# Performance work log

Hardware: AMD Instinct MI355X
Metric: run time of the kernel (lower is better)

Reference implementation:

```python
import jax, jax.numpy as jnp
import numpy as np

OUT_FEAT = 32  # output_feature; projected dim = OUT_FEAT**2 = 1024
D_K = OUT_FEAT ** 0.5  # NOTE: source divides by sqrt(output_feature), not sqrt(output_feature^2)


def setup_inputs() -> dict:
    key = jax.random.key(0)
    ks = jax.random.split(key, 7)
    N, D_in, D_proj = 4096, 1024, OUT_FEAT * OUT_FEAT
    s = 1.0 / np.sqrt(D_in)
    return {
        "x": jax.random.normal(ks[0], (N, D_in), jnp.float32),
        "Wq": jax.random.normal(ks[1], (D_in, D_proj), jnp.float32) * s,
        "bq": jax.random.normal(ks[2], (D_proj,), jnp.float32) * s,
        "Wk": jax.random.normal(ks[3], (D_in, D_proj), jnp.float32) * s,
        "bk": jax.random.normal(ks[4], (D_proj,), jnp.float32) * s,
        "Wv": jax.random.normal(ks[5], (D_in, D_proj), jnp.float32) * s,
        "bv": jax.random.normal(ks[6], (D_proj,), jnp.float32) * s,
    }


def reference(x, Wq, bq, Wk, bk, Wv, bv):
    # QKV projections: [N, D_proj]
    Q = x @ Wq + bq
    K = x @ Wk + bk
    V = x @ Wv + bv
    # scores: [N, N], scaled by sqrt(output_feature) per the source
    scores = (Q @ K.T) / D_K
    attn_weights = jax.nn.softmax(scores, axis=-1)
    attn_output = attn_weights @ V  # [N, D_proj]
    attn_output = attn_output.reshape(-1, OUT_FEAT, OUT_FEAT)  # mode='cov' reshape
    return attn_output, attn_weights
```

## Files before the change

### kernel.cpp

```cpp
#include <hip/hip_runtime.h>

typedef short short8 __attribute__((ext_vector_type(8)));
typedef float f32x4 __attribute__((ext_vector_type(4)));

constexpr int NROW  = 4096;
constexpr int DIN   = 1024;
constexpr int DPROJ = 1024;
constexpr float INV_DK = 0.17677669529663687f;

__device__ __forceinline__ unsigned short f2bf(float f) {
  union { float f; unsigned int u; } v; v.f = f;
  unsigned int r = v.u + 0x7FFFu + ((v.u >> 16) & 1u);
  return (unsigned short)(r >> 16);
}
__device__ __forceinline__ float bf2f(unsigned short h) {
  union { unsigned int u; float f; } v; v.u = ((unsigned int)h) << 16; return v.f;
}

template<int KB>
__device__ __forceinline__ void stage_tile(const unsigned short* __restrict__ g,
                                           long row0, long ldK, long k0,
                                           unsigned short* lds_tile, int w, int lane) {
  if constexpr (KB == 64) {
    const int rsub = lane >> 3;
    const int csw  = ((lane & 7) ^ (rsub & 7)) * 8;
#pragma unroll
    for (int it = 0; it < 4; ++it) {
      const int rowblk = w * 32 + it * 8;
      const unsigned short* src = g + (row0 + rowblk + rsub) * ldK + k0 + csw;
      unsigned short* dst = lds_tile + rowblk * 64;
      __builtin_amdgcn_global_load_lds(
          (const __attribute__((address_space(1))) unsigned int*)(const void*)src,
          (__attribute__((address_space(3))) unsigned int*)(void*)dst, 16, 0, 0);
    }
  } else {
    const int rsub = lane >> 2;
    const int csw  = ((lane & 3) ^ ((rsub >> 1) & 3)) * 8;
#pragma unroll
    for (int it = 0; it < 2; ++it) {
      const int rowblk = w * 32 + it * 16;
      const unsigned short* src = g + (row0 + rowblk + rsub) * ldK + k0 + csw;
      unsigned short* dst = lds_tile + rowblk * 32;
      __builtin_amdgcn_global_load_lds(
          (const __attribute__((address_space(1))) unsigned int*)(const void*)src,
          (__attribute__((address_space(3))) unsigned int*)(void*)dst, 16, 0, 0);
    }
  }
}

__device__ __forceinline__ void stage_tile64r(const unsigned short* __restrict__ g,
                                              long row0, long ldK, long k0,
                                              unsigned short* lds_tile, int w, int lane) {
  const int rsub = lane >> 3;
  const int csw  = ((lane & 7) ^ (rsub & 7)) * 8;
#pragma unroll
  for (int it = 0; it < 2; ++it) {
    const int rowblk = w * 16 + it * 8;
    const unsigned short* src = g + (row0 + rowblk + rsub) * ldK + k0 + csw;
    unsigned short* dst = lds_tile + rowblk * 64;
    __builtin_amdgcn_global_load_lds(
        (const __attribute__((address_space(1))) unsigned int*)(const void*)src,
        (__attribute__((address_space(3))) unsigned int*)(void*)dst, 16, 0, 0);
  }
}

__global__ __launch_bounds__(256, 2) void qk_proj(
    const unsigned short* __restrict__ xh, const unsigned short* __restrict__ xl,
    const unsigned short* __restrict__ WqTh, const unsigned short* __restrict__ WqTl,
    const unsigned short* __restrict__ WkTh, const unsigned short* __restrict__ WkTl,
    const float* __restrict__ bq, const float* __restrict__ bk,
    unsigned short* __restrict__ Qh, unsigned short* __restrict__ Ql,
    unsigned short* __restrict__ Kh, unsigned short* __restrict__ Kl)
{
  constexpr int K = 1024, N = 1024, TS = 128 * 32;
  __shared__ __align__(16) unsigned short lds[2][4 * TS];
  const int tid = threadIdx.x, w = tid >> 6, lane = tid & 63;
  const int wr = w >> 1, wc = w & 1, lrow = lane & 15, lgrp = lane >> 4;
  const int which = blockIdx.x >> 8;
  const int b = blockIdx.x & 255;
  const long bm = (long)(b >> 3) * 128;
  const long bn = (long)(b & 7) * 128;
  const unsigned short* Bh = which ? WkTh : WqTh;
  const unsigned short* Bl = which ? WkTl : WqTl;
  const float* bias = which ? bk : bq;
  unsigned short* Oh = which ? Kh : Qh;
  unsigned short* Ol = which ? Kl : Ql;

  f32x4 acc[4][4] = {};
  const int nsteps = K >> 5;

  stage_tile<32>(xh, bm, K, 0, &lds[0][0 * TS], w, lane);
  stage_tile<32>(Bh, bn, K, 0, &lds[0][1 * TS], w, lane);
  stage_tile<32>(xl, bm, K, 0, &lds[0][2 * TS], w, lane);
  stage_tile<32>(Bl, bn, K, 0, &lds[0][3 * TS], w, lane);

  int cur = 0;
  for (int t = 0; t < nsteps; ++t) {
    __syncthreads();
    if (t + 1 < nsteps) {
      const long k0 = (long)(t + 1) << 5;
      const int nb = cur ^ 1;
      stage_tile<32>(xh, bm, K, k0, &lds[nb][0 * TS], w, lane);
      stage_tile<32>(Bh, bn, K, k0, &lds[nb][1 * TS], w, lane);
      stage_tile<32>(xl, bm, K, k0, &lds[nb][2 * TS], w, lane);
      stage_tile<32>(Bl, bn, K, k0, &lds[nb][3 * TS], w, lane);
    }
    const unsigned short* L = lds[cur];
    short8 ah[4], bh[4], al[4], bl[4];
#pragma unroll
    for (int i = 0; i < 4; ++i) {
      const int ra = wr * 64 + i * 16 + lrow;
      const int offa = ra * 32 + ((lgrp ^ ((ra >> 1) & 3)) * 8);
      ah[i] = *(const short8*)&L[0 * TS + offa];
      al[i] = *(const short8*)&L[2 * TS + offa];
      const int rb = wc * 64 + i * 16 + lrow;
      const int offb = rb * 32 + ((lgrp ^ ((rb >> 1) & 3)) * 8);
      bh[i] = *(const short8*)&L[1 * TS + offb];
      bl[i] = *(const short8*)&L[3 * TS + offb];
    }
#pragma unroll
    for (int i = 0; i < 4; ++i)
#pragma unroll
      for (int j = 0; j < 4; ++j) {
        acc[i][j] = __builtin_amdgcn_mfma_f32_16x16x32_bf16(ah[i], bh[j], acc[i][j], 0, 0, 0);
        acc[i][j] = __builtin_amdgcn_mfma_f32_16x16x32_bf16(ah[i], bl[j], acc[i][j], 0, 0, 0);
        acc[i][j] = __builtin_amdgcn_mfma_f32_16x16x32_bf16(al[i], bh[j], acc[i][j], 0, 0, 0);
      }
    cur ^= 1;
  }

#pragma unroll
  for (int i = 0; i < 4; ++i) {
    const long rbase = bm + wr * 64 + i * 16 + lgrp * 4;
#pragma unroll
    for (int j = 0; j < 4; ++j) {
      const long cg = bn + wc * 64 + j * 16 + lrow;
#pragma unroll
      for (int r = 0; r < 4; ++r) {
        const long rg = rbase + r;
        float v = acc[i][j][r] + bias[cg];
        unsigned short h = f2bf(v);
        Oh[rg * N + cg] = h;
        Ol[rg * N + cg] = f2bf(v - bf2f(h));
      }
    }
  }
}

template<int EPI>
__global__ __launch_bounds__(256, 2) void gemm_n64(
    const unsigned short* __restrict__ A, const unsigned short* __restrict__ B,
    const float* __restrict__ bias, float* __restrict__ Cf,
    unsigned short* __restrict__ Co, int M, int N, int K)
{
  constexpr int TSA = 128 * 64;
  constexpr int TSB = 64 * 64;
  __shared__ __align__(16) unsigned short lds[2][TSA + TSB];
  const int tid = threadIdx.x, w = tid >> 6, lane = tid & 63;
  const int wr = w >> 1, wc = w & 1, lrow = lane & 15, lgrp = lane >> 4;
  const long bm = (long)blockIdx.y * 128, bn = (long)blockIdx.x * 64;

  f32x4 acc[4][2] = {};
  const int nsteps = K >> 6;

  stage_tile<64>(A, bm, K, 0, &lds[0][0], w, lane);
  stage_tile64r(B, bn, K, 0, &lds[0][TSA], w, lane);

  int cur = 0;
  for (int t = 0; t < nsteps; ++t) {
    __syncthreads();
    if (t + 1 < nsteps) {
      const long k0 = (long)(t + 1) << 6;
      const int nb = cur ^ 1;
      stage_tile<64>(A, bm, K, k0, &lds[nb][0], w, lane);
      stage_tile64r(B, bn, K, k0, &lds[nb][TSA], w, lane);
    }
    const unsigned short* L = lds[cur];
#pragma unroll
    for (int s = 0; s < 2; ++s) {
      short8 a[4], bb[2];
#pragma unroll
      for (int i = 0; i < 4; ++i) {
        const int ra = wr * 64 + i * 16 + lrow;
        const int offa = ra * 64 + (((s * 4 + lgrp) ^ (ra & 7)) * 8);
        a[i] = *(const short8*)&L[offa];
      }
#pragma unroll
      for (int j = 0; j < 2; ++j) {
        const int rb = wc * 32 + j * 16 + lrow;
        const int offb = rb * 64 + (((s * 4 + lgrp) ^ (rb & 7)) * 8);
        bb[j] = *(const short8*)&L[TSA + offb];
      }
#pragma unroll
      for (int i = 0; i < 4; ++i)
#pragma unroll
        for (int j = 0; j < 2; ++j)
          acc[i][j] = __builtin_amdgcn_mfma_f32_16x16x32_bf16(a[i], bb[j], acc[i][j], 0, 0, 0);
    }
    cur ^= 1;
  }

#pragma unroll
  for (int i = 0; i < 4; ++i) {
    const long rbase = bm + wr * 64 + i * 16 + lgrp * 4;
#pragma unroll
    for (int j = 0; j < 2; ++j) {
      const long cg = bn + wc * 32 + j * 16 + lrow;
#pragma unroll
      for (int r = 0; r < 4; ++r) {
        const long rg = rbase + r;
        if constexpr (EPI == 0) {
          Cf[rg * (long)N + cg] = acc[i][j][r];
        } else {
          Co[rg * (long)N + cg] = f2bf(acc[i][j][r] + bias[rg]);
        }
      }
    }
  }
}

__device__ __forceinline__ void stage256(const unsigned short* __restrict__ g,
    long row0, long ldK, long k0, unsigned short* tile, int w, int lane, int rnd)
{
  const int row_in = rnd * 128 + w * 16 + (lane >> 2);
  const int csw = ((lane & 3) ^ ((row_in >> 1) & 3)) * 8;
  const unsigned short* src = g + (row0 + row_in) * ldK + k0 + csw;
  unsigned short* dst = tile + (rnd * 128 + w * 16) * 32;
  __builtin_amdgcn_global_load_lds(
      (const __attribute__((address_space(1))) unsigned int*)(const void*)src,
      (__attribute__((address_space(3))) unsigned int*)(void*)dst, 16, 0, 0);
}

__global__ __launch_bounds__(512, 2) void score_gemm256(
    const unsigned short* __restrict__ Ah, const unsigned short* __restrict__ Al,
    const unsigned short* __restrict__ Bh, const unsigned short* __restrict__ Bl,
    float* __restrict__ Cf, int M, int N, int K, float alpha)
{
  __shared__ __align__(16) unsigned short lds[2][4 * 8192];
  const int tid  = threadIdx.x;
  const int w    = tid >> 6, lane = tid & 63;
  const int wr   = w >> 2,   wc   = w & 3;
  const int lrow = lane & 15, lgrp = lane >> 4;
  const long bm = (long)blockIdx.y * 256, bn = (long)blockIdx.x * 256;

  f32x4 acc[8][4] = {};
  const int nsteps = K >> 5;

  {
    unsigned short* B0 = &lds[0][0];
#pragma unroll
    for (int r = 0; r < 2; ++r) {
      stage256(Ah, bm, K, 0, B0 + 0 * 8192, w, lane, r);
      stage256(Al, bm, K, 0, B0 + 1 * 8192, w, lane, r);
      stage256(Bh, bn, K, 0, B0 + 2 * 8192, w, lane, r);
      stage256(Bl, bn, K, 0, B0 + 3 * 8192, w, lane, r);
    }
  }
  asm volatile("s_waitcnt vmcnt(0)" ::: "memory");

  int cur = 0;
  for (int t = 0; t < nsteps; ++t) {
    const unsigned short* L = &lds[cur][0];
    unsigned short* Ln = &lds[cur ^ 1][0];
    const long kn = (long)(t + 1) << 5;
    const bool pf = (t + 1 < nsteps);
#pragma unroll
    for (int q = 0; q < 4; ++q) {
      __builtin_amdgcn_s_barrier();
      __builtin_amdgcn_sched_barrier(0);
      const int mh = q >> 1, nh = q & 1;
      short8 a_h[4], a_l[4], b_h[2], b_l[2];
#pragma unroll
      for (int i = 0; i < 4; ++i) {
        const int ra = wr * 128 + mh * 64 + i * 16 + lrow;
        const int offa = ra * 32 + ((lgrp ^ ((ra >> 1) & 3)) * 8);
        a_h[i] = *(const short8*)&L[0 * 8192 + offa];
        a_l[i] = *(const short8*)&L[1 * 8192 + offa];
      }
#pragma unroll
      for (int j = 0; j < 2; ++j) {
        const int rb = wc * 64 + nh * 32 + j * 16 + lrow;
        const int offb = rb * 32 + ((lgrp ^ ((rb >> 1) & 3)) * 8);
        b_h[j] = *(const short8*)&L[2 * 8192 + offb];
        b_l[j] = *(const short8*)&L[3 * 8192 + offb];
      }
      if (pf && q == 0) {
#pragma unroll
        for (int r = 0; r < 2; ++r) {
          stage256(Ah, bm, K, kn, Ln + 0 * 8192, w, lane, r);
          stage256(Bh, bn, K, kn, Ln + 2 * 8192, w, lane, r);
        }
      }
      if (pf && q == 1) {
#pragma unroll
        for (int r = 0; r < 2; ++r) {
          stage256(Al, bm, K, kn, Ln + 1 * 8192, w, lane, r);
          stage256(Bl, bn, K, kn, Ln + 3 * 8192, w, lane, r);
        }
      }
      __builtin_amdgcn_sched_barrier(0);
      __builtin_amdgcn_s_setprio(1);
#pragma unroll
      for (int i = 0; i < 4; ++i)
#pragma unroll
        for (int j = 0; j < 2; ++j) {
          const int ai = mh * 4 + i, aj = nh * 2 + j;
          acc[ai][aj] = __builtin_amdgcn_mfma_f32_16x16x32_bf16(a_h[i], b_h[j], acc[ai][aj], 0, 0, 0);
          acc[ai][aj] = __builtin_amdgcn_mfma_f32_16x16x32_bf16(a_h[i], b_l[j], acc[ai][aj], 0, 0, 0);
          acc[ai][aj] = __builtin_amdgcn_mfma_f32_16x16x32_bf16(a_l[i], b_h[j], acc[ai][aj], 0, 0, 0);
        }
      __builtin_amdgcn_s_setprio(0);
      if (q == 3) {
        asm volatile("s_waitcnt vmcnt(0)" ::: "memory");
        __builtin_amdgcn_sched_barrier(0);
      }
    }
    cur ^= 1;
  }

#pragma unroll
  for (int i = 0; i < 8; ++i) {
    const long rbase = bm + wr * 128 + i * 16 + lgrp * 4;
#pragma unroll
    for (int j = 0; j < 4; ++j) {
      const long cg = bn + wc * 64 + j * 16 + lrow;
#pragma unroll
      for (int r = 0; r < 4; ++r)
        Cf[(rbase + r) * (long)N + cg] = alpha * acc[i][j][r];
    }
  }
}

__global__ __launch_bounds__(256) void split_rows(const float* __restrict__ in,
    unsigned short* __restrict__ oh, unsigned short* __restrict__ ol, int n4)
{
  int idx = blockIdx.x * 256 + threadIdx.x;
  const int stride = gridDim.x * 256;
  for (; idx < n4; idx += stride) {
    float4 v = ((const float4*)in)[idx];
    ushort4 h, l;
    h.x = f2bf(v.x); l.x = f2bf(v.x - bf2f(h.x));
    h.y = f2bf(v.y); l.y = f2bf(v.y - bf2f(h.y));
    h.z = f2bf(v.z); l.z = f2bf(v.z - bf2f(h.z));
    h.w = f2bf(v.w); l.w = f2bf(v.w - bf2f(h.w));
    ((ushort4*)oh)[idx] = h;
    ((ushort4*)ol)[idx] = l;
  }
}

__global__ __launch_bounds__(256) void split_transpose(const float* __restrict__ W,
    unsigned short* __restrict__ oTh, unsigned short* __restrict__ oTl, int R, int C)
{
  __shared__ float t[64][65];
  const int rt = blockIdx.y * 64, ct = blockIdx.x * 64;
  const int r0 = threadIdx.x >> 4, c4 = (threadIdx.x & 15) * 4;
#pragma unroll
  for (int rr = 0; rr < 4; ++rr) {
    const int row = r0 + rr * 16;
    float4 v = *(const float4*)(W + (long)(rt + row) * C + ct + c4);
    t[row][c4 + 0] = v.x; t[row][c4 + 1] = v.y;
    t[row][c4 + 2] = v.z; t[row][c4 + 3] = v.w;
  }
  __syncthreads();
#pragma unroll
  for (int rr = 0; rr < 4; ++rr) {
    const int orow = r0 + rr * 16;
    float x0 = t[c4 + 0][orow], x1 = t[c4 + 1][orow];
    float x2 = t[c4 + 2][orow], x3 = t[c4 + 3][orow];
    ushort4 h, l;
    h.x = f2bf(x0); l.x = f2bf(x0 - bf2f(h.x));
    h.y = f2bf(x1); l.y = f2bf(x1 - bf2f(h.y));
    h.z = f2bf(x2); l.z = f2bf(x2 - bf2f(h.z));
    h.w = f2bf(x3); l.w = f2bf(x3 - bf2f(h.w));
    *(ushort4*)(oTh + (long)(ct + orow) * R + rt + c4) = h;
    *(ushort4*)(oTl + (long)(ct + orow) * R + rt + c4) = l;
  }
}

__global__ __launch_bounds__(256) void softmax_p(float* __restrict__ S,
                                                 unsigned short* __restrict__ P)
{
  const int tid = threadIdx.x;
  float* p = S + (size_t)blockIdx.x * 4096;
  unsigned short* pb = P + (size_t)blockIdx.x * 4096;
  float4 v[4];
  float mx = -3.402823466e38f;
#pragma unroll
  for (int i = 0; i < 4; ++i) {
    v[i] = *(const float4*)(p + 4 * (tid + i * 256));
    mx = fmaxf(mx, fmaxf(fmaxf(v[i].x, v[i].y), fmaxf(v[i].z, v[i].w)));
  }
#pragma unroll
  for (int off = 32; off >= 1; off >>= 1) mx = fmaxf(mx, __shfl_xor(mx, off));
  __shared__ float redm[4], reds[4];
  if ((tid & 63) == 0) redm[tid >> 6] = mx;
  __syncthreads();
  mx = fmaxf(fmaxf(redm[0], redm[1]), fmaxf(redm[2], redm[3]));

  float sum = 0.f;
#pragma unroll
  for (int i = 0; i < 4; ++i) {
    v[i].x = __expf(v[i].x - mx); v[i].y = __expf(v[i].y - mx);
    v[i].z = __expf(v[i].z - mx); v[i].w = __expf(v[i].w - mx);
    sum += (v[i].x + v[i].y) + (v[i].z + v[i].w);
  }
#pragma unroll
  for (int off = 32; off >= 1; off >>= 1) sum += __shfl_xor(sum, off);
  if ((tid & 63) == 0) reds[tid >> 6] = sum;
  __syncthreads();
  sum = (reds[0] + reds[1]) + (reds[2] + reds[3]);
  const float inv = 1.0f / sum;
#pragma unroll
  for (int i = 0; i < 4; ++i) {
    v[i].x *= inv; v[i].y *= inv; v[i].z *= inv; v[i].w *= inv;
    *(float4*)(p + 4 * (tid + i * 256)) = v[i];
    ushort4 h;
    h.x = f2bf(v[i].x); h.y = f2bf(v[i].y); h.z = f2bf(v[i].z); h.w = f2bf(v[i].w);
    *(ushort4*)(pb + 4 * (tid + i * 256)) = h;
  }
}

extern "C" void kernel_launch(void* const* d_in, const int* in_sizes, int n_in,
                              void* d_out, int out_size, void* d_ws, size_t ws_size,
                              hipStream_t stream)
{
  const float* x  = (const float*)d_in[0];
  const float* Wq = (const float*)d_in[1];
  const float* bq = (const float*)d_in[2];
  const float* Wk = (const float*)d_in[3];
  const float* bk = (const float*)d_in[4];
  const float* Wv = (const float*)d_in[5];
  const float* bv = (const float*)d_in[6];

  float* attn_out = (float*)d_out;
  float* attn_w   = attn_out + (size_t)NROW * DPROJ;

  constexpr size_t MB = 1ull << 20;
  char* sc = (char*)attn_w;
  unsigned short* xh   = (unsigned short*)(sc + 0 * MB);
  unsigned short* xl   = (unsigned short*)(sc + 8 * MB);
  unsigned short* WqTh = (unsigned short*)(sc + 16 * MB);
  unsigned short* WqTl = (unsigned short*)(sc + 18 * MB);
  unsigned short* WkTh = (unsigned short*)(sc + 20 * MB);
  unsigned short* WkTl = (unsigned short*)(sc + 22 * MB);
  unsigned short* WvTh = (unsigned short*)(sc + 24 * MB);
  unsigned short* WvTl = (unsigned short*)(sc + 26 * MB);
  char* wsb = (char*)d_ws;
  unsigned short* VT = (unsigned short*)(wsb + 0 * MB);
  unsigned short* Qh = (unsigned short*)(wsb + 8 * MB);
  unsigned short* Ql = (unsigned short*)(wsb + 16 * MB);
  unsigned short* Kh = (unsigned short*)(wsb + 24 * MB);
  unsigned short* Kl = (unsigned short*)(wsb + 32 * MB);
  unsigned short* P  = (unsigned short*)(wsb + 8 * MB);

  dim3 blk(256);

  split_rows<<<4096, blk, 0, stream>>>(x, xh, xl, NROW * DIN / 4);
  dim3 gtr(16, 16);
  split_transpose<<<gtr, blk, 0, stream>>>(Wq, WqTh, WqTl, DIN, DPROJ);
  split_transpose<<<gtr, blk, 0, stream>>>(Wk, WkTh, WkTl, DIN, DPROJ);
  split_transpose<<<gtr, blk, 0, stream>>>(Wv, WvTh, WvTl, DIN, DPROJ);

  gemm_n64<3><<<dim3(NROW / 64, DPROJ / 128), blk, 0, stream>>>(
      WvTh, xh, bv, nullptr, VT, DPROJ, NROW, DIN);

  qk_proj<<<512, blk, 0, stream>>>(xh, xl, WqTh, WqTl, WkTh, WkTl,
                                   bq, bk, Qh, Ql, Kh, Kl);

  score_gemm256<<<dim3(NROW / 256, NROW / 256), dim3(512), 0, stream>>>(
      Qh, Ql, Kh, Kl, attn_w, NROW, NROW, DPROJ, INV_DK);

  softmax_p<<<NROW, blk, 0, stream>>>(attn_w, P);

  gemm_n64<0><<<dim3(DPROJ / 64, NROW / 128), blk, 0, stream>>>(
      P, VT, nullptr, attn_out, nullptr, NROW, DPROJ, NROW);
}
```

Measured before the change: 238.4 us.

## Restructure score GEMM main loop: issue all prefetches upfront, keep B fragments resident

Moves all four global-to-LDS prefetches for the next K step to the start of each iteration instead of splitting them across the first two quarter-phases. B fragments are loaded from LDS once per K step and kept in registers, while A fragments are streamed in four phases of two row tiles each. This cuts redundant B reads from LDS and gives the async loads more time to overlap. In exchange it raises register pressure and issues the prefetches in one burst.

```diff
diff --git a/kernel.cpp b/kernel.cpp
--- a/kernel.cpp
+++ b/kernel.cpp
@@ -246,15 +246,12 @@
   f32x4 acc[8][4] = {};
   const int nsteps = K >> 5;
 
-  {
-    unsigned short* B0 = &lds[0][0];
-#pragma unroll
-    for (int r = 0; r < 2; ++r) {
-      stage256(Ah, bm, K, 0, B0 + 0 * 8192, w, lane, r);
-      stage256(Al, bm, K, 0, B0 + 1 * 8192, w, lane, r);
-      stage256(Bh, bn, K, 0, B0 + 2 * 8192, w, lane, r);
-      stage256(Bl, bn, K, 0, B0 + 3 * 8192, w, lane, r);
-    }
+#pragma unroll
+  for (int r = 0; r < 2; ++r) {
+    stage256(Ah, bm, K, 0, &lds[0][0 * 8192], w, lane, r);
+    stage256(Al, bm, K, 0, &lds[0][1 * 8192], w, lane, r);
+    stage256(Bh, bn, K, 0, &lds[0][2 * 8192], w, lane, r);
+    stage256(Bl, bn, K, 0, &lds[0][3 * 8192], w, lane, r);
   }
   asm volatile("s_waitcnt vmcnt(0)" ::: "memory");
 
@@ -264,57 +261,59 @@
     unsigned short* Ln = &lds[cur ^ 1][0];
     const long kn = (long)(t + 1) << 5;
     const bool pf = (t + 1 < nsteps);
-#pragma unroll
-    for (int q = 0; q < 4; ++q) {
-      __builtin_amdgcn_s_barrier();
-      __builtin_amdgcn_sched_barrier(0);
-      const int mh = q >> 1, nh = q & 1;
-      short8 a_h[4], a_l[4], b_h[2], b_l[2];
-#pragma unroll
-      for (int i = 0; i < 4; ++i) {
-        const int ra = wr * 128 + mh * 64 + i * 16 + lrow;
+
+    __builtin_amdgcn_s_barrier();
+    __builtin_amdgcn_sched_barrier(0);
+
+    if (pf) {
+#pragma unroll
+      for (int r = 0; r < 2; ++r) {
+        stage256(Ah, bm, K, kn, Ln + 0 * 8192, w, lane, r);
+        stage256(Al, bm, K, kn, Ln + 1 * 8192, w, lane, r);
+        stage256(Bh, bn, K, kn, Ln + 2 * 8192, w, lane, r);
+        stage256(Bl, bn, K, kn, Ln + 3 * 8192, w, lane, r);
+      }
+    }
+
+    short8 b_h[4], b_l[4];
+#pragma unroll
+    for (int j = 0; j < 4; ++j) {
+      const int rb = wc * 64 + j * 16 + lrow;
+      const int offb = rb * 32 + ((lgrp ^ ((rb >> 1) & 3)) * 8);
+      b_h[j] = *(const short8*)&L[2 * 8192 + offb];
+      b_l[j] = *(const short8*)&L[3 * 8192 + offb];
+    }
+
+#pragma unroll
+    for (int p = 0; p < 4; ++p) {
+      if (p) {
+        __builtin_amdgcn_sched_barrier(0);
+        __builtin_amdgcn_s_barrier();
+        __builtin_amdgcn_sched_barrier(0);
+      }
+      short8 a_h[2], a_l[2];
+#pragma unroll
+      for (int i = 0; i < 2; ++i) {
+        const int ra = wr * 128 + (p * 2 + i) * 16 + lrow;
         const int offa = ra * 32 + ((lgrp ^ ((ra >> 1) & 3)) * 8);
         a_h[i] = *(const short8*)&L[0 * 8192 + offa];
         a_l[i] = *(const short8*)&L[1 * 8192 + offa];
       }
-#pragma unroll
-      for (int j = 0; j < 2; ++j) {
-        const int rb = wc * 64 + nh * 32 + j * 16 + lrow;
-        const int offb = rb * 32 + ((lgrp ^ ((rb >> 1) & 3)) * 8);
-        b_h[j] = *(const short8*)&L[2 * 8192 + offb];
-        b_l[j] = *(const short8*)&L[3 * 8192 + offb];
-      }
-      if (pf && q == 0) {
-#pragma unroll
-        for (int r = 0; r < 2; ++r) {
-          stage256(Ah, bm, K, kn, Ln + 0 * 8192, w, lane, r);
-          stage256(Bh, bn, K, kn, Ln + 2 * 8192, w, lane, r);
-        }
-      }
-      if (pf && q == 1) {
-#pragma unroll
-        for (int r = 0; r < 2; ++r) {
-          stage256(Al, bm, K, kn, Ln + 1 * 8192, w, lane, r);
-          stage256(Bl, bn, K, kn, Ln + 3 * 8192, w, lane, r);
-        }
-      }
-      __builtin_amdgcn_sched_barrier(0);
       __builtin_amdgcn_s_setprio(1);
 #pragma unroll
-      for (int i = 0; i < 4; ++i)
-#pragma unroll
-        for (int j = 0; j < 2; ++j) {
-          const int ai = mh * 4 + i, aj = nh * 2 + j;
-          acc[ai][aj] = __builtin_amdgcn_mfma_f32_16x16x32_bf16(a_h[i], b_h[j], acc[ai][aj], 0, 0, 0);
-          acc[ai][aj] = __builtin_amdgcn_mfma_f32_16x16x32_bf16(a_h[i], b_l[j], acc[ai][aj], 0, 0, 0);
-          acc[ai][aj] = __builtin_amdgcn_mfma_f32_16x16x32_bf16(a_l[i], b_h[j], acc[ai][aj], 0, 0, 0);
+      for (int i = 0; i < 2; ++i)
+#pragma unroll
+        for (int j = 0; j < 4; ++j) {
+          const int ai = p * 2 + i;
+          acc[ai][j] = __builtin_amdgcn_mfma_f32_16x16x32_bf16(a_h[i], b_h[j], acc[ai][j], 0, 0, 0);
+          acc[ai][j] = __builtin_amdgcn_mfma_f32_16x16x32_bf16(a_h[i], b_l[j], acc[ai][j], 0, 0, 0);
+          acc[ai][j] = __builtin_amdgcn_mfma_f32_16x16x32_bf16(a_l[i], b_h[j], acc[ai][j], 0, 0, 0);
         }
       __builtin_amdgcn_s_setprio(0);
-      if (q == 3) {
-        asm volatile("s_waitcnt vmcnt(0)" ::: "memory");
-        __builtin_amdgcn_sched_barrier(0);
-      }
-    }
+    }
+
+    __builtin_amdgcn_sched_barrier(0);
+    asm volatile("s_waitcnt vmcnt(0)" ::: "memory");
     cur ^= 1;
   }
 
```

After: 239.8 us. No clear change (+0.6%).
